# Kernel tuning notes

Hardware: AMD Instinct MI355X
Metric: run time of the kernel (lower is better)

Reference implementation:

```python
import jax, jax.numpy as jnp
import numpy as np

B, S, D = 2, 2048, 1024
H = 16
HD = D // H

def setup_inputs() -> dict:
    key = jax.random.key(0)
    k1, k2, k3 = jax.random.split(key, 3)
    # xavier-uniform-ish scale for weights
    x = jax.random.normal(k1, (B, S, D), dtype=jnp.float32)
    lim_qkv = np.sqrt(6.0 / (D + 3 * D)).astype(np.float32)
    lim_o = np.sqrt(6.0 / (D + D)).astype(np.float32)
    qkv_w = jax.random.uniform(k2, (3 * D, D), minval=-lim_qkv, maxval=lim_qkv, dtype=jnp.float32)
    o_w = jax.random.uniform(k3, (D, D), minval=-lim_o, maxval=lim_o, dtype=jnp.float32)
    qkv_b = jnp.zeros((3 * D,), dtype=jnp.float32)
    o_b = jnp.zeros((D,), dtype=jnp.float32)
    return {"x": x, "qkv_w": qkv_w, "qkv_b": qkv_b, "o_w": o_w, "o_b": o_b}

def reference(x, qkv_w, qkv_b, o_w, o_b):
    b, s, _ = x.shape
    # qkv projection: Linear(input_dim, 3*embed_dim)
    qkv = jnp.einsum('bsd,ed->bse', x, qkv_w) + qkv_b          # [B,S,3D]
    qkv = qkv.reshape(b, s, H, 3 * HD).transpose(0, 2, 1, 3)    # [B,H,S,3*HD]
    q, k, v = jnp.split(qkv, 3, axis=-1)                        # each [B,H,S,HD]
    scale = 1.0 / np.sqrt(HD).astype(np.float32)
    scores = jnp.einsum('bhqd,bhkd->bhqk', q, k) * scale        # [B,H,S,S]
    attn = jax.nn.softmax(scores, axis=-1)
    vals = jnp.einsum('bhqk,bhkd->bhqd', attn, v)               # [B,H,S,HD]
    vals = vals.transpose(0, 2, 1, 3).reshape(b, s, H * HD)     # [B,S,D]
    o = jnp.einsum('bse,de->bsd', vals, o_w) + o_b              # [B,S,D]
    return o
```

## Files before the change

kernel.cpp:

```cpp
#include <hip/hip_runtime.h>
#include <math.h>
#include <stdint.h>

typedef _Float16 half_t;
typedef _Float16 f16x8 __attribute__((ext_vector_type(8)));
typedef _Float16 f16x4 __attribute__((ext_vector_type(4)));
typedef _Float16 f16x2 __attribute__((ext_vector_type(2)));
typedef float    f32x4 __attribute__((ext_vector_type(4)));
typedef float    f32x16 __attribute__((ext_vector_type(16)));
typedef unsigned int u32x2 __attribute__((ext_vector_type(2)));

__device__ __forceinline__ void gload16(const void* g, void* l) {
    __builtin_amdgcn_global_load_lds(
        (const __attribute__((address_space(1))) void*)(uintptr_t)g,
        (__attribute__((address_space(3))) void*)(uint32_t)(uintptr_t)l,
        16, 0, 0);
}

__device__ __forceinline__ float fast_exp2(float x) {
#if __has_builtin(__builtin_amdgcn_exp2f)
    return __builtin_amdgcn_exp2f(x);
#else
    return exp2f(x);
#endif
}
__device__ __forceinline__ unsigned cvt2h_u32(float a, float b) {
#if __has_builtin(__builtin_amdgcn_cvt_pkrtz)
    union { __fp16 __attribute__((ext_vector_type(2))) s; unsigned d; } u;
    u.s = __builtin_amdgcn_cvt_pkrtz(a, b);
    return u.d;
#else
    union { f16x2 s; unsigned d; } u;
    u.s = (f16x2){ (half_t)a, (half_t)b };
    return u.d;
#endif
}

#define QSCALE 0.18033688011112042f

__global__ __launch_bounds__(256)
void cvt3_kernel(const float* __restrict__ a, half_t* __restrict__ da, int na,
                 const float* __restrict__ b, half_t* __restrict__ db, int nb,
                 const float* __restrict__ c, half_t* __restrict__ dc)
{
    int i = blockIdx.x * 256 + threadIdx.x;
    const float* s; half_t* d; int off;
    if (i < na)           { s = a; d = da; off = i; }
    else if (i < na + nb) { s = b; d = db; off = i - na; }
    else                  { s = c; d = dc; off = i - na - nb; }
    float4 v = reinterpret_cast<const float4*>(s)[off];
    f16x4 h = { (half_t)v.x, (half_t)v.y, (half_t)v.z, (half_t)v.w };
    reinterpret_cast<f16x4*>(d)[off] = h;
}

template<int BM, int BN, int MODE, int MINWG>
__global__ __launch_bounds__(256, MINWG)
void gemm_kernel(const half_t* __restrict__ A,
                 const half_t* __restrict__ Bw,
                 const float* __restrict__ bias,
                 void* __restrict__ outp,
                 half_t* __restrict__ kout,
                 half_t* __restrict__ vtout,
                 int N, int K, int nbx)
{
    constexpr int CA = BM / 32, CB = BN / 32;
    constexpr int MW = BM / 2,  NW = BN / 2;
    constexpr int IF = MW / 16, JF = NW / 16;
    constexpr int AE = BM * 64, BE = BN * 64;

    __shared__ half_t As[2][AE];
    __shared__ half_t Bs[2][BE];

    const int tid  = threadIdx.x;
    const int lane = tid & 63;
    const int w    = tid >> 6;
    const int wm   = w >> 1, wn = w & 1;
    const int lr   = lane & 15, lg = lane >> 4;

    const int nwg = gridDim.x;
    const int cpx = nwg >> 3;
    const int swz = (blockIdx.x & 7) * cpx + (blockIdx.x >> 3);
    const int m0  = (swz % nbx) * BM;
    const int n0  = (swz / nbx) * BN;

    const int srow = lane >> 3;
    const int scol = (lane & 7) * 8;

    f32x4 acc[JF][IF] = {};

    const int NT = K >> 6;

    #pragma unroll
    for (int c = 0; c < CA; ++c) {
        const int chunk = w * CA + c;
        const int row   = chunk * 8 + srow;
        gload16(&A[(size_t)(m0 + row) * K + scol], &As[0][chunk * 512]);
    }
    #pragma unroll
    for (int c = 0; c < CB; ++c) {
        const int chunk = w * CB + c;
        const int row   = chunk * 8 + srow;
        gload16(&Bw[(size_t)(n0 + row) * K + scol], &Bs[0][chunk * 512]);
    }
    __syncthreads();

    int cur = 0;
    for (int kt = 0; kt < NT; ++kt) {
        if (kt + 1 < NT) {
            const int k1 = (kt + 1) << 6;
            #pragma unroll
            for (int c = 0; c < CA; ++c) {
                const int chunk = w * CA + c;
                const int row   = chunk * 8 + srow;
                gload16(&A[(size_t)(m0 + row) * K + k1 + scol], &As[cur ^ 1][chunk * 512]);
            }
            #pragma unroll
            for (int c = 0; c < CB; ++c) {
                const int chunk = w * CB + c;
                const int row   = chunk * 8 + srow;
                gload16(&Bw[(size_t)(n0 + row) * K + k1 + scol], &Bs[cur ^ 1][chunk * 512]);
            }
        }

        #pragma unroll
        for (int kk = 0; kk < 2; ++kk) {
            f16x8 af[IF], bf[JF];
            #pragma unroll
            for (int i = 0; i < IF; ++i)
                af[i] = *reinterpret_cast<const f16x8*>(&As[cur][(wm*MW + i*16 + lr) * 64 + kk*32 + lg*8]);
            #pragma unroll
            for (int j = 0; j < JF; ++j)
                bf[j] = *reinterpret_cast<const f16x8*>(&Bs[cur][(wn*NW + j*16 + lr) * 64 + kk*32 + lg*8]);
            #pragma unroll
            for (int j = 0; j < JF; ++j)
                #pragma unroll
                for (int i = 0; i < IF; ++i)
                    acc[j][i] = __builtin_amdgcn_mfma_f32_16x16x32_f16(bf[j], af[i], acc[j][i], 0, 0, 0);
        }

        if (kt + 1 < NT) __syncthreads();
        cur ^= 1;
    }

    #pragma unroll
    for (int j = 0; j < JF; ++j) {
        const int nb = n0 + wn*NW + j*16 + lg*4;
        const float4 bv = *reinterpret_cast<const float4*>(&bias[nb]);
        #pragma unroll
        for (int i = 0; i < IF; ++i) {
            const int gm = m0 + wm*MW + i*16 + lr;
            f32x4 v = acc[j][i];
            v[0] += bv.x; v[1] += bv.y; v[2] += bv.z; v[3] += bv.w;
            if (MODE == 1) {
                float4 st = { v[0], v[1], v[2], v[3] };
                *reinterpret_cast<float4*>(&((float*)outp)[(size_t)gm * N + nb]) = st;
            } else {
                const int b = gm >> 11, s = gm & 2047;
                const int h = nb / 192, cc = nb % 192;
                const int t = cc >> 6, d = cc & 63;
                const size_t bh = (size_t)(b * 16 + h);
                if (t == 0) {
                    f16x4 hv = { (half_t)(v[0]*QSCALE), (half_t)(v[1]*QSCALE),
                                 (half_t)(v[2]*QSCALE), (half_t)(v[3]*QSCALE) };
                    *reinterpret_cast<f16x4*>(&((half_t*)outp)[(bh*2048 + s)*64 + d]) = hv;
                } else if (t == 1) {
                    f16x4 hv = { (half_t)v[0], (half_t)v[1], (half_t)v[2], (half_t)v[3] };
                    *reinterpret_cast<f16x4*>(&kout[(bh*2048 + s)*64 + d]) = hv;
                } else {
                    #pragma unroll
                    for (int r = 0; r < 4; ++r)
                        vtout[(bh*64 + d + r)*2048 + s] = (half_t)v[r];
                }
            }
        }
    }
}

__global__ __launch_bounds__(512, 2)
void attn_kernel(const half_t* __restrict__ qb,
                 const half_t* __restrict__ kb,
                 const half_t* __restrict__ vtb,
                 half_t* __restrict__ vals)
{
    __shared__ char buf[49152];
    half_t* KtH = (half_t*)buf;
    half_t* VtH = (half_t*)(buf + 24576);

    const int tid  = threadIdx.x;
    const int lane = tid & 63;
    const int w    = tid >> 6;
    const int wq   = w & 3;
    const int kh   = w >> 2;
    const int q32  = lane & 31;
    const int hi   = lane >> 5;
    const int i    = blockIdx.x;
    const int bh   = (i & 7) * 4 + ((i >> 3) & 3);
    const int qblk = i >> 5;
    const int b    = bh >> 4, h = bh & 15;
    const size_t base = (size_t)bh * 2048 * 64;
    const int q0 = qblk * 128;
    const int swk = lane & 7;

    f16x8 qf[4];
    {
        const int qr = q0 + wq*32 + q32;
        #pragma unroll
        for (int kd = 0; kd < 4; ++kd)
            qf[kd] = *reinterpret_cast<const f16x8*>(&qb[base + (size_t)qr*64 + kd*16 + hi*8]);
    }

    const int srow = tid >> 3;
    const int ssl  = (tid & 7) ^ (srow & 7);
    const half_t* kg = kb  + base + (size_t)srow * 64   + ssl * 8;
    const half_t* vg = vtb + base + (size_t)srow * 2048 + ssl * 8;
    const int ldst = w * 512;

    f32x16 acco[2] = {};
    float l_run = 0.0f;

    #pragma unroll
    for (int tt = 0; tt < 3; ++tt) {
        gload16(kg + (size_t)tt * 4096, &KtH[tt * 4096 + ldst]);
        gload16(vg + tt * 64,           &VtH[tt * 4096 + ldst]);
    }

    int bi = 0;
    for (int t = 0; t < 32; ++t) {
        const int rem = 31 - t;
        if (rem >= 2)      asm volatile("s_waitcnt vmcnt(4)" ::: "memory");
        else if (rem == 1) asm volatile("s_waitcnt vmcnt(2)" ::: "memory");
        else               asm volatile("s_waitcnt vmcnt(0)" ::: "memory");
        __builtin_amdgcn_s_barrier();
        __builtin_amdgcn_sched_barrier(0);

        const half_t* Kc = &KtH[bi * 4096];
        const half_t* Vc = &VtH[bi * 4096];

        f32x16 accs = {};
        __builtin_amdgcn_s_setprio(1);
        #pragma unroll
        for (int kd = 0; kd < 4; ++kd) {
            const f16x8 kf = *reinterpret_cast<const f16x8*>(
                &Kc[(kh*32 + q32) * 64 + (((kd*2 + hi) ^ swk) << 3)]);
            accs = __builtin_amdgcn_mfma_f32_32x32x16_f16(kf, qf[kd], accs, 0, 0, 0);
        }
        __builtin_amdgcn_s_setprio(0);

        unsigned P2[8];
        float psum = 0.0f;
        #pragma unroll
        for (int p = 0; p < 8; ++p) {
            const float pa = fast_exp2(accs[2*p]);
            const float pb = fast_exp2(accs[2*p+1]);
            psum += pa + pb;
            P2[p] = cvt2h_u32(pa, pb);
        }
        l_run += psum;

        __builtin_amdgcn_s_setprio(1);
        #pragma unroll
        for (int kb2 = 0; kb2 < 2; ++kb2) {
            const u32x2 s0 = __builtin_amdgcn_permlane32_swap(P2[4*kb2+0], P2[4*kb2+2], false, false);
            const u32x2 s1 = __builtin_amdgcn_permlane32_swap(P2[4*kb2+1], P2[4*kb2+3], false, false);
            union { unsigned u[4]; f16x8 v; } pf;
            pf.u[0] = s0[0]; pf.u[1] = s1[0]; pf.u[2] = s0[1]; pf.u[3] = s1[1];
            #pragma unroll
            for (int d2 = 0; d2 < 2; ++d2) {
                const f16x8 vf = *reinterpret_cast<const f16x8*>(
                    &Vc[(d2*32 + q32) * 64 + (((kh*4 + kb2*2 + hi) ^ swk) << 3)]);
                acco[d2] = __builtin_amdgcn_mfma_f32_32x32x16_f16(vf, pf.v, acco[d2], 0, 0, 0);
            }
        }
        __builtin_amdgcn_s_setprio(0);

        __builtin_amdgcn_s_barrier();
        if (t < 29) {
            gload16(kg + (size_t)(t + 3) * 4096, &KtH[bi * 4096 + ldst]);
            gload16(vg + (t + 3) * 64,           &VtH[bi * 4096 + ldst]);
        }
        bi = (bi == 2) ? 0 : bi + 1;
    }

    l_run += __shfl_xor(l_run, 32);

    float* mrg = (float*)buf;
    __syncthreads();
    if (kh == 1) {
        float* dst = &mrg[(wq*64 + lane) * 33];
        #pragma unroll
        for (int d2 = 0; d2 < 2; ++d2)
            #pragma unroll
            for (int r = 0; r < 16; ++r) dst[d2*16 + r] = acco[d2][r];
        dst[32] = l_run;
    }
    __syncthreads();
    if (kh == 0) {
        const float* src = &mrg[(wq*64 + lane) * 33];
        const float inv_l = 1.0f / (l_run + src[32]);
        const int row = b*2048 + q0 + wq*32 + q32;
        #pragma unroll
        for (int d2 = 0; d2 < 2; ++d2) {
            #pragma unroll
            for (int rq = 0; rq < 4; ++rq) {
                const int dbase = d2*32 + rq*8 + hi*4;
                f16x4 hv;
                #pragma unroll
                for (int j = 0; j < 4; ++j) {
                    const int r = rq*4 + j;
                    hv[j] = (half_t)((acco[d2][r] + src[d2*16 + r]) * inv_l);
                }
                *reinterpret_cast<f16x4*>(&vals[(size_t)row*1024 + h*64 + dbase]) = hv;
            }
        }
    }
}

extern "C" void kernel_launch(void* const* d_in, const int* in_sizes, int n_in,
                              void* d_out, int out_size, void* d_ws, size_t ws_size,
                              hipStream_t stream)
{
    const float* x     = (const float*)d_in[0];
    const float* qkv_w = (const float*)d_in[1];
    const float* qkv_b = (const float*)d_in[2];
    const float* o_w   = (const float*)d_in[3];
    const float* o_b   = (const float*)d_in[4];
    float* out = (float*)d_out;

    const size_t M1 = (size_t)1024 * 1024;
    half_t* x16   = (half_t*)d_ws;
    half_t* w16   = x16   + 4 * M1;
    half_t* ow16  = w16   + 3 * M1;
    half_t* qbuf  = ow16  + 1 * M1;
    half_t* kbuf  = qbuf  + 4 * M1;
    half_t* vtbuf = kbuf  + 4 * M1;
    half_t* vals  = vtbuf + 4 * M1;

    cvt3_kernel<<<8192, 256, 0, stream>>>(x, x16, 1048576, qkv_w, w16, 786432, o_w, ow16);
    gemm_kernel<128, 128, 0, 2><<<768, 256, 0, stream>>>(
        x16, w16, qkv_b, qbuf, kbuf, vtbuf, 3072, 1024, 32);
    attn_kernel<<<512, 512, 0, stream>>>(qbuf, kbuf, vtbuf, vals);
    gemm_kernel<128, 64, 1, 2><<<512, 256, 0, stream>>>(
        vals, ow16, o_b, out, nullptr, nullptr, 1024, 1024, 32);
}
```

Measured before the change: 114.0 us.

## Double query rows per attention warp and single-buffer the QKV GEMM

Each attention wave now handles two 32-row query chunks against the same K/V tiles. This halves the grid to 256 blocks and reuses each LDS K/V fragment for twice the MFMA work, at the cost of more registers (launch bound drops to 1 block per CU). The QKV projection GEMM gets an optional single-buffered path with sync-load-compute per K tile, aiming for 3 workgroups per CU through lower LDS use. This gives up load/compute overlap in exchange for occupancy. The output GEMM keeps double buffering.

```diff
diff --git a/kernel.cpp b/kernel.cpp
--- a/kernel.cpp
+++ b/kernel.cpp
@@ -53,7 +53,7 @@
     reinterpret_cast<f16x4*>(d)[off] = h;
 }
 
-template<int BM, int BN, int MODE, int MINWG>
+template<int BM, int BN, int MODE, int MINWG, int DBUF>
 __global__ __launch_bounds__(256, MINWG)
 void gemm_kernel(const half_t* __restrict__ A,
                  const half_t* __restrict__ Bw,
@@ -67,9 +67,10 @@
     constexpr int MW = BM / 2,  NW = BN / 2;
     constexpr int IF = MW / 16, JF = NW / 16;
     constexpr int AE = BM * 64, BE = BN * 64;
-
-    __shared__ half_t As[2][AE];
-    __shared__ half_t Bs[2][BE];
+    constexpr int NB = DBUF ? 2 : 1;
+
+    __shared__ half_t As[NB * AE];
+    __shared__ half_t Bs[NB * BE];
 
     const int tid  = threadIdx.x;
     const int lane = tid & 63;
@@ -88,58 +89,90 @@
 
     f32x4 acc[JF][IF] = {};
 
-    const int NT = K >> 6;
-
-    #pragma unroll
-    for (int c = 0; c < CA; ++c) {
-        const int chunk = w * CA + c;
-        const int row   = chunk * 8 + srow;
-        gload16(&A[(size_t)(m0 + row) * K + scol], &As[0][chunk * 512]);
-    }
-    #pragma unroll
-    for (int c = 0; c < CB; ++c) {
-        const int chunk = w * CB + c;
-        const int row   = chunk * 8 + srow;
-        gload16(&Bw[(size_t)(n0 + row) * K + scol], &Bs[0][chunk * 512]);
-    }
-    __syncthreads();
-
-    int cur = 0;
-    for (int kt = 0; kt < NT; ++kt) {
-        if (kt + 1 < NT) {
-            const int k1 = (kt + 1) << 6;
+    if constexpr (!DBUF) {
+        for (int k0 = 0; k0 < K; k0 += 64) {
             #pragma unroll
             for (int c = 0; c < CA; ++c) {
                 const int chunk = w * CA + c;
                 const int row   = chunk * 8 + srow;
-                gload16(&A[(size_t)(m0 + row) * K + k1 + scol], &As[cur ^ 1][chunk * 512]);
+                gload16(&A[(size_t)(m0 + row) * K + k0 + scol], &As[chunk * 512]);
             }
             #pragma unroll
             for (int c = 0; c < CB; ++c) {
                 const int chunk = w * CB + c;
                 const int row   = chunk * 8 + srow;
-                gload16(&Bw[(size_t)(n0 + row) * K + k1 + scol], &Bs[cur ^ 1][chunk * 512]);
-            }
-        }
-
-        #pragma unroll
-        for (int kk = 0; kk < 2; ++kk) {
-            f16x8 af[IF], bf[JF];
-            #pragma unroll
-            for (int i = 0; i < IF; ++i)
-                af[i] = *reinterpret_cast<const f16x8*>(&As[cur][(wm*MW + i*16 + lr) * 64 + kk*32 + lg*8]);
-            #pragma unroll
-            for (int j = 0; j < JF; ++j)
-                bf[j] = *reinterpret_cast<const f16x8*>(&Bs[cur][(wn*NW + j*16 + lr) * 64 + kk*32 + lg*8]);
-            #pragma unroll
-            for (int j = 0; j < JF; ++j)
+                gload16(&Bw[(size_t)(n0 + row) * K + k0 + scol], &Bs[chunk * 512]);
+            }
+            __syncthreads();
+
+            #pragma unroll
+            for (int kk = 0; kk < 2; ++kk) {
+                f16x8 af[IF], bf[JF];
                 #pragma unroll
                 for (int i = 0; i < IF; ++i)
-                    acc[j][i] = __builtin_amdgcn_mfma_f32_16x16x32_f16(bf[j], af[i], acc[j][i], 0, 0, 0);
-        }
-
-        if (kt + 1 < NT) __syncthreads();
-        cur ^= 1;
+                    af[i] = *reinterpret_cast<const f16x8*>(&As[(wm*MW + i*16 + lr) * 64 + kk*32 + lg*8]);
+                #pragma unroll
+                for (int j = 0; j < JF; ++j)
+                    bf[j] = *reinterpret_cast<const f16x8*>(&Bs[(wn*NW + j*16 + lr) * 64 + kk*32 + lg*8]);
+                #pragma unroll
+                for (int j = 0; j < JF; ++j)
+                    #pragma unroll
+                    for (int i = 0; i < IF; ++i)
+                        acc[j][i] = __builtin_amdgcn_mfma_f32_16x16x32_f16(bf[j], af[i], acc[j][i], 0, 0, 0);
+            }
+            __syncthreads();
+        }
+    } else {
+        const int NT = K >> 6;
+        #pragma unroll
+        for (int c = 0; c < CA; ++c) {
+            const int chunk = w * CA + c;
+            const int row   = chunk * 8 + srow;
+            gload16(&A[(size_t)(m0 + row) * K + scol], &As[chunk * 512]);
+        }
+        #pragma unroll
+        for (int c = 0; c < CB; ++c) {
+            const int chunk = w * CB + c;
+            const int row   = chunk * 8 + srow;
+            gload16(&Bw[(size_t)(n0 + row) * K + scol], &Bs[chunk * 512]);
+        }
+        __syncthreads();
+
+        int cur = 0;
+        for (int kt = 0; kt < NT; ++kt) {
+            if (kt + 1 < NT) {
+                const int k1 = (kt + 1) << 6;
+                #pragma unroll
+                for (int c = 0; c < CA; ++c) {
+                    const int chunk = w * CA + c;
+                    const int row   = chunk * 8 + srow;
+                    gload16(&A[(size_t)(m0 + row) * K + k1 + scol], &As[(cur ^ 1) * AE + chunk * 512]);
+                }
+                #pragma unroll
+                for (int c = 0; c < CB; ++c) {
+                    const int chunk = w * CB + c;
+                    const int row   = chunk * 8 + srow;
+                    gload16(&Bw[(size_t)(n0 + row) * K + k1 + scol], &Bs[(cur ^ 1) * BE + chunk * 512]);
+                }
+            }
+            #pragma unroll
+            for (int kk = 0; kk < 2; ++kk) {
+                f16x8 af[IF], bf[JF];
+                #pragma unroll
+                for (int i = 0; i < IF; ++i)
+                    af[i] = *reinterpret_cast<const f16x8*>(&As[cur * AE + (wm*MW + i*16 + lr) * 64 + kk*32 + lg*8]);
+                #pragma unroll
+                for (int j = 0; j < JF; ++j)
+                    bf[j] = *reinterpret_cast<const f16x8*>(&Bs[cur * BE + (wn*NW + j*16 + lr) * 64 + kk*32 + lg*8]);
+                #pragma unroll
+                for (int j = 0; j < JF; ++j)
+                    #pragma unroll
+                    for (int i = 0; i < IF; ++i)
+                        acc[j][i] = __builtin_amdgcn_mfma_f32_16x16x32_f16(bf[j], af[i], acc[j][i], 0, 0, 0);
+            }
+            if (kt + 1 < NT) __syncthreads();
+            cur ^= 1;
+        }
     }
 
     #pragma unroll
@@ -176,13 +209,13 @@
     }
 }
 
-__global__ __launch_bounds__(512, 2)
+__global__ __launch_bounds__(512, 1)
 void attn_kernel(const half_t* __restrict__ qb,
                  const half_t* __restrict__ kb,
                  const half_t* __restrict__ vtb,
                  half_t* __restrict__ vals)
 {
-    __shared__ char buf[49152];
+    __shared__ __attribute__((aligned(16))) char buf[49152];
     half_t* KtH = (half_t*)buf;
     half_t* VtH = (half_t*)(buf + 24576);
 
@@ -198,15 +231,16 @@
     const int qblk = i >> 5;
     const int b    = bh >> 4, h = bh & 15;
     const size_t base = (size_t)bh * 2048 * 64;
-    const int q0 = qblk * 128;
+    const int q0 = qblk * 256 + wq * 64;
     const int swk = lane & 7;
 
-    f16x8 qf[4];
-    {
-        const int qr = q0 + wq*32 + q32;
+    f16x8 qf[2][4];
+    #pragma unroll
+    for (int qc = 0; qc < 2; ++qc) {
+        const int qr = q0 + qc*32 + q32;
         #pragma unroll
         for (int kd = 0; kd < 4; ++kd)
-            qf[kd] = *reinterpret_cast<const f16x8*>(&qb[base + (size_t)qr*64 + kd*16 + hi*8]);
+            qf[qc][kd] = *reinterpret_cast<const f16x8*>(&qb[base + (size_t)qr*64 + kd*16 + hi*8]);
     }
 
     const int srow = tid >> 3;
@@ -215,8 +249,8 @@
     const half_t* vg = vtb + base + (size_t)srow * 2048 + ssl * 8;
     const int ldst = w * 512;
 
-    f32x16 acco[2] = {};
-    float l_run = 0.0f;
+    f32x16 acco[2][2] = {};
+    float l_run[2] = {0.f, 0.f};
 
     #pragma unroll
     for (int tt = 0; tt < 3; ++tt) {
@@ -236,39 +270,47 @@
         const half_t* Kc = &KtH[bi * 4096];
         const half_t* Vc = &VtH[bi * 4096];
 
-        f32x16 accs = {};
+        f32x16 accs[2] = {};
         __builtin_amdgcn_s_setprio(1);
         #pragma unroll
         for (int kd = 0; kd < 4; ++kd) {
             const f16x8 kf = *reinterpret_cast<const f16x8*>(
                 &Kc[(kh*32 + q32) * 64 + (((kd*2 + hi) ^ swk) << 3)]);
-            accs = __builtin_amdgcn_mfma_f32_32x32x16_f16(kf, qf[kd], accs, 0, 0, 0);
+            accs[0] = __builtin_amdgcn_mfma_f32_32x32x16_f16(kf, qf[0][kd], accs[0], 0, 0, 0);
+            accs[1] = __builtin_amdgcn_mfma_f32_32x32x16_f16(kf, qf[1][kd], accs[1], 0, 0, 0);
         }
         __builtin_amdgcn_s_setprio(0);
 
-        unsigned P2[8];
-        float psum = 0.0f;
-        #pragma unroll
-        for (int p = 0; p < 8; ++p) {
-            const float pa = fast_exp2(accs[2*p]);
-            const float pb = fast_exp2(accs[2*p+1]);
-            psum += pa + pb;
-            P2[p] = cvt2h_u32(pa, pb);
-        }
-        l_run += psum;
+        unsigned P2[2][8];
+        #pragma unroll
+        for (int qc = 0; qc < 2; ++qc) {
+            float psum = 0.0f;
+            #pragma unroll
+            for (int p = 0; p < 8; ++p) {
+                const float pa = fast_exp2(accs[qc][2*p]);
+                const float pb = fast_exp2(accs[qc][2*p+1]);
+                psum += pa + pb;
+                P2[qc][p] = cvt2h_u32(pa, pb);
+            }
+            l_run[qc] += psum;
+        }
 
         __builtin_amdgcn_s_setprio(1);
         #pragma unroll
         for (int kb2 = 0; kb2 < 2; ++kb2) {
-            const u32x2 s0 = __builtin_amdgcn_permlane32_swap(P2[4*kb2+0], P2[4*kb2+2], false, false);
-            const u32x2 s1 = __builtin_amdgcn_permlane32_swap(P2[4*kb2+1], P2[4*kb2+3], false, false);
-            union { unsigned u[4]; f16x8 v; } pf;
-            pf.u[0] = s0[0]; pf.u[1] = s1[0]; pf.u[2] = s0[1]; pf.u[3] = s1[1];
+            const u32x2 s0a = __builtin_amdgcn_permlane32_swap(P2[0][4*kb2+0], P2[0][4*kb2+2], false, false);
+            const u32x2 s1a = __builtin_amdgcn_permlane32_swap(P2[0][4*kb2+1], P2[0][4*kb2+3], false, false);
+            const u32x2 s0b = __builtin_amdgcn_permlane32_swap(P2[1][4*kb2+0], P2[1][4*kb2+2], false, false);
+            const u32x2 s1b = __builtin_amdgcn_permlane32_swap(P2[1][4*kb2+1], P2[1][4*kb2+3], false, false);
+            union { unsigned u[4]; f16x8 v; } pfa, pfb;
+            pfa.u[0] = s0a[0]; pfa.u[1] = s1a[0]; pfa.u[2] = s0a[1]; pfa.u[3] = s1a[1];
+            pfb.u[0] = s0b[0]; pfb.u[1] = s1b[0]; pfb.u[2] = s0b[1]; pfb.u[3] = s1b[1];
             #pragma unroll
             for (int d2 = 0; d2 < 2; ++d2) {
                 const f16x8 vf = *reinterpret_cast<const f16x8*>(
                     &Vc[(d2*32 + q32) * 64 + (((kh*4 + kb2*2 + hi) ^ swk) << 3)]);
-                acco[d2] = __builtin_amdgcn_mfma_f32_32x32x16_f16(vf, pf.v, acco[d2], 0, 0, 0);
+                acco[0][d2] = __builtin_amdgcn_mfma_f32_32x32x16_f16(vf, pfa.v, acco[0][d2], 0, 0, 0);
+                acco[1][d2] = __builtin_amdgcn_mfma_f32_32x32x16_f16(vf, pfb.v, acco[1][d2], 0, 0, 0);
             }
         }
         __builtin_amdgcn_s_setprio(0);
@@ -281,35 +323,39 @@
         bi = (bi == 2) ? 0 : bi + 1;
     }
 
-    l_run += __shfl_xor(l_run, 32);
+    l_run[0] += __shfl_xor(l_run[0], 32);
+    l_run[1] += __shfl_xor(l_run[1], 32);
 
     float* mrg = (float*)buf;
-    __syncthreads();
-    if (kh == 1) {
-        float* dst = &mrg[(wq*64 + lane) * 33];
-        #pragma unroll
-        for (int d2 = 0; d2 < 2; ++d2)
-            #pragma unroll
-            for (int r = 0; r < 16; ++r) dst[d2*16 + r] = acco[d2][r];
-        dst[32] = l_run;
-    }
-    __syncthreads();
-    if (kh == 0) {
-        const float* src = &mrg[(wq*64 + lane) * 33];
-        const float inv_l = 1.0f / (l_run + src[32]);
-        const int row = b*2048 + q0 + wq*32 + q32;
-        #pragma unroll
-        for (int d2 = 0; d2 < 2; ++d2) {
-            #pragma unroll
-            for (int rq = 0; rq < 4; ++rq) {
-                const int dbase = d2*32 + rq*8 + hi*4;
-                f16x4 hv;
-                #pragma unroll
-                for (int j = 0; j < 4; ++j) {
-                    const int r = rq*4 + j;
-                    hv[j] = (half_t)((acco[d2][r] + src[d2*16 + r]) * inv_l);
+    #pragma unroll
+    for (int qc = 0; qc < 2; ++qc) {
+        __syncthreads();
+        if (kh == 1) {
+            float* dst = &mrg[(wq*64 + lane) * 33];
+            #pragma unroll
+            for (int d2 = 0; d2 < 2; ++d2)
+                #pragma unroll
+                for (int r = 0; r < 16; ++r) dst[d2*16 + r] = acco[qc][d2][r];
+            dst[32] = l_run[qc];
+        }
+        __syncthreads();
+        if (kh == 0) {
+            const float* src = &mrg[(wq*64 + lane) * 33];
+            const float inv_l = 1.0f / (l_run[qc] + src[32]);
+            const int row = b*2048 + q0 + qc*32 + q32;
+            #pragma unroll
+            for (int d2 = 0; d2 < 2; ++d2) {
+                #pragma unroll
+                for (int rq = 0; rq < 4; ++rq) {
+                    const int dbase = d2*32 + rq*8 + hi*4;
+                    f16x4 hv;
+                    #pragma unroll
+                    for (int j = 0; j < 4; ++j) {
+                        const int r = rq*4 + j;
+                        hv[j] = (half_t)((acco[qc][d2][r] + src[d2*16 + r]) * inv_l);
+                    }
+                    *reinterpret_cast<f16x4*>(&vals[(size_t)row*1024 + h*64 + dbase]) = hv;
                 }
-                *reinterpret_cast<f16x4*>(&vals[(size_t)row*1024 + h*64 + dbase]) = hv;
             }
         }
     }
@@ -336,9 +382,9 @@
     half_t* vals  = vtbuf + 4 * M1;
 
     cvt3_kernel<<<8192, 256, 0, stream>>>(x, x16, 1048576, qkv_w, w16, 786432, o_w, ow16);
-    gemm_kernel<128, 128, 0, 2><<<768, 256, 0, stream>>>(
+    gemm_kernel<128, 128, 0, 3, 0><<<768, 256, 0, stream>>>(
         x16, w16, qkv_b, qbuf, kbuf, vtbuf, 3072, 1024, 32);
-    attn_kernel<<<512, 512, 0, stream>>>(qbuf, kbuf, vtbuf, vals);
-    gemm_kernel<128, 64, 1, 2><<<512, 256, 0, stream>>>(
+    attn_kernel<<<256, 512, 0, stream>>>(qbuf, kbuf, vtbuf, vals);
+    gemm_kernel<128, 64, 1, 2, 1><<<512, 256, 0, stream>>>(
         vals, ow16, o_b, out, nullptr, nullptr, 1024, 1024, 32);
 }
```

Result: faster. 109.4 us (-4.0%).

## Use single-buffered smaller-tile QKV GEMM with higher occupancy and XCD-aware mapping

Applied to the files above, without the earlier changes.

Adds template switches for double buffering and block mapping to the GEMM. The QKV projection now runs with 128x64 tiles, a single LDS buffer, a min-waves hint of 6, and a mapping that gives each XCD a contiguous group of M tiles. The goal is to hide latency through more resident workgroups instead of software double buffering, and to improve L2 reuse of the A rows within each XCD. The cost is an extra barrier per K step with no overlap inside a block, plus doubled grid size and more redundant A reads.

```diff
diff --git a/kernel.cpp b/kernel.cpp
--- a/kernel.cpp
+++ b/kernel.cpp
@@ -53,7 +53,7 @@
     reinterpret_cast<f16x4*>(d)[off] = h;
 }
 
-template<int BM, int BN, int MODE, int MINWG>
+template<int BM, int BN, int MODE, int MINWG, int DBUF, int MAP>
 __global__ __launch_bounds__(256, MINWG)
 void gemm_kernel(const half_t* __restrict__ A,
                  const half_t* __restrict__ Bw,
@@ -67,9 +67,10 @@
     constexpr int MW = BM / 2,  NW = BN / 2;
     constexpr int IF = MW / 16, JF = NW / 16;
     constexpr int AE = BM * 64, BE = BN * 64;
-
-    __shared__ half_t As[2][AE];
-    __shared__ half_t Bs[2][BE];
+    constexpr int NB = DBUF ? 2 : 1;
+
+    __shared__ half_t As[NB * AE];
+    __shared__ half_t Bs[NB * BE];
 
     const int tid  = threadIdx.x;
     const int lane = tid & 63;
@@ -77,69 +78,109 @@
     const int wm   = w >> 1, wn = w & 1;
     const int lr   = lane & 15, lg = lane >> 4;
 
-    const int nwg = gridDim.x;
-    const int cpx = nwg >> 3;
-    const int swz = (blockIdx.x & 7) * cpx + (blockIdx.x >> 3);
-    const int m0  = (swz % nbx) * BM;
-    const int n0  = (swz / nbx) * BN;
+    int m0, n0;
+    if constexpr (MAP == 1) {
+        const int xcd = blockIdx.x & 7;
+        const int c   = blockIdx.x >> 3;
+        m0 = (xcd * 4 + (c & 3)) * BM;
+        n0 = (c >> 2) * BN;
+    } else {
+        const int nwg = gridDim.x;
+        const int cpx = nwg >> 3;
+        const int swz = (blockIdx.x & 7) * cpx + (blockIdx.x >> 3);
+        m0 = (swz % nbx) * BM;
+        n0 = (swz / nbx) * BN;
+    }
 
     const int srow = lane >> 3;
     const int scol = (lane & 7) * 8;
 
     f32x4 acc[JF][IF] = {};
 
-    const int NT = K >> 6;
-
-    #pragma unroll
-    for (int c = 0; c < CA; ++c) {
-        const int chunk = w * CA + c;
-        const int row   = chunk * 8 + srow;
-        gload16(&A[(size_t)(m0 + row) * K + scol], &As[0][chunk * 512]);
-    }
-    #pragma unroll
-    for (int c = 0; c < CB; ++c) {
-        const int chunk = w * CB + c;
-        const int row   = chunk * 8 + srow;
-        gload16(&Bw[(size_t)(n0 + row) * K + scol], &Bs[0][chunk * 512]);
-    }
-    __syncthreads();
-
-    int cur = 0;
-    for (int kt = 0; kt < NT; ++kt) {
-        if (kt + 1 < NT) {
-            const int k1 = (kt + 1) << 6;
+    if constexpr (!DBUF) {
+        for (int k0 = 0; k0 < K; k0 += 64) {
             #pragma unroll
             for (int c = 0; c < CA; ++c) {
                 const int chunk = w * CA + c;
                 const int row   = chunk * 8 + srow;
-                gload16(&A[(size_t)(m0 + row) * K + k1 + scol], &As[cur ^ 1][chunk * 512]);
+                gload16(&A[(size_t)(m0 + row) * K + k0 + scol], &As[chunk * 512]);
             }
             #pragma unroll
             for (int c = 0; c < CB; ++c) {
                 const int chunk = w * CB + c;
                 const int row   = chunk * 8 + srow;
-                gload16(&Bw[(size_t)(n0 + row) * K + k1 + scol], &Bs[cur ^ 1][chunk * 512]);
-            }
-        }
-
-        #pragma unroll
-        for (int kk = 0; kk < 2; ++kk) {
-            f16x8 af[IF], bf[JF];
-            #pragma unroll
-            for (int i = 0; i < IF; ++i)
-                af[i] = *reinterpret_cast<const f16x8*>(&As[cur][(wm*MW + i*16 + lr) * 64 + kk*32 + lg*8]);
-            #pragma unroll
-            for (int j = 0; j < JF; ++j)
-                bf[j] = *reinterpret_cast<const f16x8*>(&Bs[cur][(wn*NW + j*16 + lr) * 64 + kk*32 + lg*8]);
-            #pragma unroll
-            for (int j = 0; j < JF; ++j)
+                gload16(&Bw[(size_t)(n0 + row) * K + k0 + scol], &Bs[chunk * 512]);
+            }
+            __syncthreads();
+
+            #pragma unroll
+            for (int kk = 0; kk < 2; ++kk) {
+                f16x8 af[IF], bf[JF];
                 #pragma unroll
                 for (int i = 0; i < IF; ++i)
-                    acc[j][i] = __builtin_amdgcn_mfma_f32_16x16x32_f16(bf[j], af[i], acc[j][i], 0, 0, 0);
-        }
-
-        if (kt + 1 < NT) __syncthreads();
-        cur ^= 1;
+                    af[i] = *reinterpret_cast<const f16x8*>(&As[(wm*MW + i*16 + lr) * 64 + kk*32 + lg*8]);
+                #pragma unroll
+                for (int j = 0; j < JF; ++j)
+                    bf[j] = *reinterpret_cast<const f16x8*>(&Bs[(wn*NW + j*16 + lr) * 64 + kk*32 + lg*8]);
+                #pragma unroll
+                for (int j = 0; j < JF; ++j)
+                    #pragma unroll
+                    for (int i = 0; i < IF; ++i)
+                        acc[j][i] = __builtin_amdgcn_mfma_f32_16x16x32_f16(bf[j], af[i], acc[j][i], 0, 0, 0);
+            }
+            __syncthreads();
+        }
+    } else {
+        const int NT = K >> 6;
+        #pragma unroll
+        for (int c = 0; c < CA; ++c) {
+            const int chunk = w * CA + c;
+            const int row   = chunk * 8 + srow;
+            gload16(&A[(size_t)(m0 + row) * K + scol], &As[chunk * 512]);
+        }
+        #pragma unroll
+        for (int c = 0; c < CB; ++c) {
+            const int chunk = w * CB + c;
+            const int row   = chunk * 8 + srow;
+            gload16(&Bw[(size_t)(n0 + row) * K + scol], &Bs[chunk * 512]);
+        }
+        __syncthreads();
+
+        int cur = 0;
+        for (int kt = 0; kt < NT; ++kt) {
+            if (kt + 1 < NT) {
+                const int k1 = (kt + 1) << 6;
+                #pragma unroll
+                for (int c = 0; c < CA; ++c) {
+                    const int chunk = w * CA + c;
+                    const int row   = chunk * 8 + srow;
+                    gload16(&A[(size_t)(m0 + row) * K + k1 + scol], &As[(cur ^ 1) * AE + chunk * 512]);
+                }
+                #pragma unroll
+                for (int c = 0; c < CB; ++c) {
+                    const int chunk = w * CB + c;
+                    const int row   = chunk * 8 + srow;
+                    gload16(&Bw[(size_t)(n0 + row) * K + k1 + scol], &Bs[(cur ^ 1) * BE + chunk * 512]);
+                }
+            }
+            #pragma unroll
+            for (int kk = 0; kk < 2; ++kk) {
+                f16x8 af[IF], bf[JF];
+                #pragma unroll
+                for (int i = 0; i < IF; ++i)
+                    af[i] = *reinterpret_cast<const f16x8*>(&As[cur * AE + (wm*MW + i*16 + lr) * 64 + kk*32 + lg*8]);
+                #pragma unroll
+                for (int j = 0; j < JF; ++j)
+                    bf[j] = *reinterpret_cast<const f16x8*>(&Bs[cur * BE + (wn*NW + j*16 + lr) * 64 + kk*32 + lg*8]);
+                #pragma unroll
+                for (int j = 0; j < JF; ++j)
+                    #pragma unroll
+                    for (int i = 0; i < IF; ++i)
+                        acc[j][i] = __builtin_amdgcn_mfma_f32_16x16x32_f16(bf[j], af[i], acc[j][i], 0, 0, 0);
+            }
+            if (kt + 1 < NT) __syncthreads();
+            cur ^= 1;
+        }
     }
 
     #pragma unroll
@@ -182,7 +223,7 @@
                  const half_t* __restrict__ vtb,
                  half_t* __restrict__ vals)
 {
-    __shared__ char buf[49152];
+    __shared__ __attribute__((aligned(16))) char buf[49152];
     half_t* KtH = (half_t*)buf;
     half_t* VtH = (half_t*)(buf + 24576);
 
@@ -336,9 +377,9 @@
     half_t* vals  = vtbuf + 4 * M1;
 
     cvt3_kernel<<<8192, 256, 0, stream>>>(x, x16, 1048576, qkv_w, w16, 786432, o_w, ow16);
-    gemm_kernel<128, 128, 0, 2><<<768, 256, 0, stream>>>(
+    gemm_kernel<128, 64, 0, 6, 0, 1><<<1536, 256, 0, stream>>>(
         x16, w16, qkv_b, qbuf, kbuf, vtbuf, 3072, 1024, 32);
     attn_kernel<<<512, 512, 0, stream>>>(qbuf, kbuf, vtbuf, vals);
-    gemm_kernel<128, 64, 1, 2><<<512, 256, 0, stream>>>(
+    gemm_kernel<128, 64, 1, 2, 1, 0><<<512, 256, 0, stream>>>(
         vals, ow16, o_b, out, nullptr, nullptr, 1024, 1024, 32);
 }
```

New measurement: 115.8 us. Within noise of the previous version (+1.6%).
